# Kernel tuning notes

Measured on AMD Instinct MI355X. Metric: run time of the kernel, lower is better.

## Reference

```python
import jax, jax.numpy as jnp
import numpy as np

T = 24
ML = 10.0   # storage capacity constant `ml` from the repo
A_PEN = 10.0  # penalty weight `A`


def setup_inputs() -> dict:
    key = jax.random.key(0)
    k1, k2 = jax.random.split(key)
    B = 1 << 20
    out = jax.random.normal(k1, (B, T), dtype=jnp.float32)
    var_y = jax.random.normal(k2, (B, 2 * T), dtype=jnp.float32)
    return {"out": out, "var_y": var_y}


def _hinge(z):
    # (sign(z)+1)/2 * |z|  ==  max(z, 0) with torch's sign/abs grad semantics
    return (jnp.sign(z) + 1.0) * 0.5 * jnp.abs(z)


def reference(out, var_y):
    p = var_y[:, :T]          # prices  [B, T]
    a = var_y[:, T:]          # demand  [B, T]
    delta = out               # control [B, T]

    # recurrent state x0 after step t is cumsum(delta); at step t the loop
    # uses the *previous* x0 (0 at t=0)
    cum = jnp.cumsum(delta, axis=1)
    x0_prev = jnp.concatenate(
        [jnp.zeros_like(delta[:, :1]), cum[:, :-1]], axis=1)  # [B, T]

    # min_value_0 term only exists for t >= 1
    t_mask = (jnp.arange(T) >= 1).astype(delta.dtype)  # [T]

    min_v0 = _hinge(-delta - a) * t_mask
    max_v1 = _hinge(-delta - x0_prev)
    min_v1 = _hinge(x0_prev + delta - ML)

    pen = (min_v0 + max_v1 + min_v1) * A_PEN
    bill = jnp.abs(a + delta) * p + pen        # [B, T]
    # loop does cost += mean_over_batch(bill_t) for each t
    cost = jnp.sum(jnp.mean(bill, axis=0))
    return cost
```

## Files before the change

kernel.cpp:

```cpp
#include <hip/hip_runtime.h>


constexpr int TT = 24;
constexpr float ML_C = 10.0f;
constexpr float A_PEN_C = 10.0f;

__global__ __launch_bounds__(256)
void pen_partial_kernel(const float* __restrict__ dout,
                        const float* __restrict__ vary,
                        float* __restrict__ partial,
                        int B, float invB) {
    const int tid = threadIdx.x;
    const int row = blockIdx.x * 256 + tid;
    float s = 0.0f;
    if (row < B) {
        const float4* o4 = reinterpret_cast<const float4*>(dout + (size_t)row * TT);
        const float4* v4 = reinterpret_cast<const float4*>(vary + (size_t)row * (2 * TT));
        float d[TT], p[TT], a[TT];
        #pragma unroll
        for (int i = 0; i < TT / 4; ++i) {
            float4 t4 = o4[i];
            d[4*i+0] = t4.x; d[4*i+1] = t4.y; d[4*i+2] = t4.z; d[4*i+3] = t4.w;
        }
        #pragma unroll
        for (int i = 0; i < TT / 4; ++i) {
            float4 t4 = v4[i];
            p[4*i+0] = t4.x; p[4*i+1] = t4.y; p[4*i+2] = t4.z; p[4*i+3] = t4.w;
        }
        #pragma unroll
        for (int i = 0; i < TT / 4; ++i) {
            float4 t4 = v4[TT / 4 + i];
            a[4*i+0] = t4.x; a[4*i+1] = t4.y; a[4*i+2] = t4.z; a[4*i+3] = t4.w;
        }
        float x0 = 0.0f;
        #pragma unroll
        for (int t = 0; t < TT; ++t) {
            const float dd = d[t];
            const float aa = a[t];
            float mv0 = fmaxf(-dd - aa, 0.0f);
            if (t == 0) mv0 = 0.0f;
            const float mx1 = fmaxf(-dd - x0, 0.0f);
            const float mv1 = fmaxf(x0 + dd - ML_C, 0.0f);
            s += fabsf(aa + dd) * p[t] + (mv0 + mx1 + mv1) * A_PEN_C;
            x0 += dd;
        }
    }
    #pragma unroll
    for (int off = 32; off > 0; off >>= 1)
        s += __shfl_down(s, off, 64);
    __shared__ float ws[4];
    if ((tid & 63) == 0) ws[tid >> 6] = s;
    __syncthreads();
    if (tid == 0) {
        partial[blockIdx.x] = (ws[0] + ws[1] + ws[2] + ws[3]) * invB;
    }
}

__global__ __launch_bounds__(256)
void pen_final_reduce_kernel(const float* __restrict__ partial,
                             float* __restrict__ out, int n) {
    const int tid = threadIdx.x;
    float s = 0.0f;
    for (int i = tid; i < n; i += 256) s += partial[i];
    #pragma unroll
    for (int off = 32; off > 0; off >>= 1)
        s += __shfl_down(s, off, 64);
    __shared__ float ws[4];
    if ((tid & 63) == 0) ws[tid >> 6] = s;
    __syncthreads();
    if (tid == 0) out[0] = ws[0] + ws[1] + ws[2] + ws[3];
}

extern "C" void kernel_launch(void* const* d_in, const int* in_sizes, int n_in,
                              void* d_out, int out_size, void* d_ws, size_t ws_size,
                              hipStream_t stream) {
    const float* dout = (const float*)d_in[0];
    const float* vary = (const float*)d_in[1];
    const int B = in_sizes[0] / TT;
    const int nblocks = (B + 255) / 256;
    float* partial = (float*)d_ws;

    pen_partial_kernel<<<nblocks, 256, 0, stream>>>(dout, vary, partial, B, 1.0f / (float)B);
    pen_final_reduce_kernel<<<1, 256, 0, stream>>>(partial, (float*)d_out, nblocks);
}
```

Measured before the change: 340.3 us.

## Stage row tiles through padded LDS for coalesced global loads

Each block now handles 64 rows with one wavefront. It loads the rows cooperatively as contiguous float4 chunks into padded shared-memory tiles, then each thread reads its own row from LDS. Before, each thread read its own strided row directly from global memory. The goal is fully coalesced global reads in place of per-thread 96/192-byte strided accesses. The cost is LDS traffic and bank behaviour from the scalar stores at odd strides, plus 4x more blocks, which makes the single-block final reduction longer.

Result: no change. 345.5 us (+1.5%).

```diff
diff --git a/kernel.cpp b/kernel.cpp
--- a/kernel.cpp
+++ b/kernel.cpp
@@ -5,55 +5,85 @@
 constexpr float ML_C = 10.0f;
 constexpr float A_PEN_C = 10.0f;
 
-__global__ __launch_bounds__(256)
+constexpr int RPB  = 64;
+constexpr int DSTR = 25;
+constexpr int VSTR = 49;
+
+__global__ __launch_bounds__(64)
 void pen_partial_kernel(const float* __restrict__ dout,
                         const float* __restrict__ vary,
                         float* __restrict__ partial,
                         int B, float invB) {
+    __shared__ float ld[RPB * DSTR];
+    __shared__ float lv[RPB * VSTR];
     const int tid = threadIdx.x;
-    const int row = blockIdx.x * 256 + tid;
+    const long long rowBase = (long long)blockIdx.x * RPB;
+
     float s = 0.0f;
-    if (row < B) {
-        const float4* o4 = reinterpret_cast<const float4*>(dout + (size_t)row * TT);
-        const float4* v4 = reinterpret_cast<const float4*>(vary + (size_t)row * (2 * TT));
-        float d[TT], p[TT], a[TT];
+
+    if (rowBase + RPB <= B) {
+        const float4* g4 = reinterpret_cast<const float4*>(dout + rowBase * TT);
         #pragma unroll
-        for (int i = 0; i < TT / 4; ++i) {
-            float4 t4 = o4[i];
-            d[4*i+0] = t4.x; d[4*i+1] = t4.y; d[4*i+2] = t4.z; d[4*i+3] = t4.w;
+        for (int i = 0; i < 6; ++i) {
+            const int f = i * RPB + tid;
+            const float4 v = g4[f];
+            const int e = 4 * f;
+            const int r = e / TT;
+            const int c = e % TT;
+            float* dst = &ld[r * DSTR + c];
+            dst[0] = v.x; dst[1] = v.y; dst[2] = v.z; dst[3] = v.w;
         }
+        const float4* h4 = reinterpret_cast<const float4*>(vary + rowBase * (2 * TT));
         #pragma unroll
-        for (int i = 0; i < TT / 4; ++i) {
-            float4 t4 = v4[i];
-            p[4*i+0] = t4.x; p[4*i+1] = t4.y; p[4*i+2] = t4.z; p[4*i+3] = t4.w;
+        for (int i = 0; i < 12; ++i) {
+            const int f = i * RPB + tid;
+            const float4 v = h4[f];
+            const int e = 4 * f;
+            const int r = e / (2 * TT);
+            const int c = e % (2 * TT);
+            float* dst = &lv[r * VSTR + c];
+            dst[0] = v.x; dst[1] = v.y; dst[2] = v.z; dst[3] = v.w;
         }
-        #pragma unroll
-        for (int i = 0; i < TT / 4; ++i) {
-            float4 t4 = v4[TT / 4 + i];
-            a[4*i+0] = t4.x; a[4*i+1] = t4.y; a[4*i+2] = t4.z; a[4*i+3] = t4.w;
-        }
+        __syncthreads();
+
+        const float* drow = &ld[tid * DSTR];
+        const float* vrow = &lv[tid * VSTR];
         float x0 = 0.0f;
         #pragma unroll
         for (int t = 0; t < TT; ++t) {
-            const float dd = d[t];
-            const float aa = a[t];
+            const float dd = drow[t];
+            const float aa = vrow[TT + t];
+            const float pp = vrow[t];
             float mv0 = fmaxf(-dd - aa, 0.0f);
             if (t == 0) mv0 = 0.0f;
             const float mx1 = fmaxf(-dd - x0, 0.0f);
             const float mv1 = fmaxf(x0 + dd - ML_C, 0.0f);
-            s += fabsf(aa + dd) * p[t] + (mv0 + mx1 + mv1) * A_PEN_C;
+            s += fabsf(aa + dd) * pp + (mv0 + mx1 + mv1) * A_PEN_C;
             x0 += dd;
         }
+    } else {
+        const long long row = rowBase + tid;
+        if (row < B) {
+            const float* drow = dout + row * TT;
+            const float* vrow = vary + row * (2 * TT);
+            float x0 = 0.0f;
+            for (int t = 0; t < TT; ++t) {
+                const float dd = drow[t];
+                const float aa = vrow[TT + t];
+                float mv0 = fmaxf(-dd - aa, 0.0f);
+                if (t == 0) mv0 = 0.0f;
+                const float mx1 = fmaxf(-dd - x0, 0.0f);
+                const float mv1 = fmaxf(x0 + dd - ML_C, 0.0f);
+                s += fabsf(aa + dd) * vrow[t] + (mv0 + mx1 + mv1) * A_PEN_C;
+                x0 += dd;
+            }
+        }
     }
+
     #pragma unroll
     for (int off = 32; off > 0; off >>= 1)
         s += __shfl_down(s, off, 64);
-    __shared__ float ws[4];
-    if ((tid & 63) == 0) ws[tid >> 6] = s;
-    __syncthreads();
-    if (tid == 0) {
-        partial[blockIdx.x] = (ws[0] + ws[1] + ws[2] + ws[3]) * invB;
-    }
+    if (tid == 0) partial[blockIdx.x] = s * invB;
 }
 
 __global__ __launch_bounds__(256)
@@ -77,9 +107,9 @@
     const float* dout = (const float*)d_in[0];
     const float* vary = (const float*)d_in[1];
     const int B = in_sizes[0] / TT;
-    const int nblocks = (B + 255) / 256;
+    const int nblocks = (B + RPB - 1) / RPB;
     float* partial = (float*)d_ws;
 
-    pen_partial_kernel<<<nblocks, 256, 0, stream>>>(dout, vary, partial, B, 1.0f / (float)B);
+    pen_partial_kernel<<<nblocks, RPB, 0, stream>>>(dout, vary, partial, B, 1.0f / (float)B);
     pen_final_reduce_kernel<<<1, 256, 0, stream>>>(partial, (float*)d_out, nblocks);
 }
```

## Split each row across four lanes with shuffle prefix scan and grid-stride loop

Applied to the files above, without the earlier changes.

Each batch row is now handled by four lanes, six timesteps each. The lanes compute the prefix of cumulative control with a two-step shuffle scan, so a wavefront's global loads hit contiguous memory instead of 96-byte and 192-byte per-thread strides. The launch becomes a fixed 1024-block grid-stride loop that walks row groups in reverse order, which also cuts the number of partial sums the final reduce has to add. The cost is extra shuffles and the narrower float2 loads.

Measured after the change: 337.5 us. Within noise of the previous version (-0.8%).

```diff
diff --git a/kernel.cpp b/kernel.cpp
--- a/kernel.cpp
+++ b/kernel.cpp
@@ -5,54 +5,82 @@
 constexpr float ML_C = 10.0f;
 constexpr float A_PEN_C = 10.0f;
 
-__global__ __launch_bounds__(256)
+constexpr int LPR = 4;
+constexpr int EPL = 6;
+constexpr int RPW = 64 / LPR;
+constexpr int NBLK = 1024;
+constexpr int NTHR = 256;
+
+__global__ __launch_bounds__(NTHR)
 void pen_partial_kernel(const float* __restrict__ dout,
                         const float* __restrict__ vary,
                         float* __restrict__ partial,
                         int B, float invB) {
-    const int tid = threadIdx.x;
-    const int row = blockIdx.x * 256 + tid;
+    const int tid  = threadIdx.x;
+    const int lane = tid & 63;
+    const int sub  = lane & (LPR - 1);
+    const int g    = lane >> 2;
+
+    const int nWaves   = gridDim.x * (NTHR / 64);
+    const int waveId   = blockIdx.x * (NTHR / 64) + (tid >> 6);
+    const int RG       = (B + RPW - 1) / RPW;
+
     float s = 0.0f;
-    if (row < B) {
-        const float4* o4 = reinterpret_cast<const float4*>(dout + (size_t)row * TT);
-        const float4* v4 = reinterpret_cast<const float4*>(vary + (size_t)row * (2 * TT));
-        float d[TT], p[TT], a[TT];
+
+    for (int it = waveId; it < RG; it += nWaves) {
+        const int rg  = RG - 1 - it;
+        const long long row = (long long)rg * RPW + g;
+        if (row >= B) continue;
+
+        const float* dp = dout + row * TT + EPL * sub;
+        const float* vp = vary + row * (2 * TT) + EPL * sub;
+        const float* ap = vp + TT;
+        float2 d01 = *(const float2*)(dp);
+        float2 d23 = *(const float2*)(dp + 2);
+        float2 d45 = *(const float2*)(dp + 4);
+        float2 p01 = *(const float2*)(vp);
+        float2 p23 = *(const float2*)(vp + 2);
+        float2 p45 = *(const float2*)(vp + 4);
+        float2 a01 = *(const float2*)(ap);
+        float2 a23 = *(const float2*)(ap + 2);
+        float2 a45 = *(const float2*)(ap + 4);
+
+        float d[EPL] = {d01.x, d01.y, d23.x, d23.y, d45.x, d45.y};
+        float p[EPL] = {p01.x, p01.y, p23.x, p23.y, p45.x, p45.y};
+        float a[EPL] = {a01.x, a01.y, a23.x, a23.y, a45.x, a45.y};
+
+        const float localsum = ((d[0] + d[1]) + (d[2] + d[3])) + (d[4] + d[5]);
+        float incl = localsum;
+        float t1 = __shfl_up(incl, 1, LPR);
+        if (sub >= 1) incl += t1;
+        float t2 = __shfl_up(incl, 2, LPR);
+        if (sub >= 2) incl += t2;
+        float x0 = incl - localsum;
+
         #pragma unroll
-        for (int i = 0; i < TT / 4; ++i) {
-            float4 t4 = o4[i];
-            d[4*i+0] = t4.x; d[4*i+1] = t4.y; d[4*i+2] = t4.z; d[4*i+3] = t4.w;
-        }
-        #pragma unroll
-        for (int i = 0; i < TT / 4; ++i) {
-            float4 t4 = v4[i];
-            p[4*i+0] = t4.x; p[4*i+1] = t4.y; p[4*i+2] = t4.z; p[4*i+3] = t4.w;
-        }
-        #pragma unroll
-        for (int i = 0; i < TT / 4; ++i) {
-            float4 t4 = v4[TT / 4 + i];
-            a[4*i+0] = t4.x; a[4*i+1] = t4.y; a[4*i+2] = t4.z; a[4*i+3] = t4.w;
-        }
-        float x0 = 0.0f;
-        #pragma unroll
-        for (int t = 0; t < TT; ++t) {
-            const float dd = d[t];
-            const float aa = a[t];
+        for (int j = 0; j < EPL; ++j) {
+            const float dd = d[j];
+            const float aa = a[j];
             float mv0 = fmaxf(-dd - aa, 0.0f);
-            if (t == 0) mv0 = 0.0f;
+            if (j == 0 && sub == 0) mv0 = 0.0f;
             const float mx1 = fmaxf(-dd - x0, 0.0f);
             const float mv1 = fmaxf(x0 + dd - ML_C, 0.0f);
-            s += fabsf(aa + dd) * p[t] + (mv0 + mx1 + mv1) * A_PEN_C;
+            s += fabsf(aa + dd) * p[j] + (mv0 + mx1 + mv1) * A_PEN_C;
             x0 += dd;
         }
     }
+
     #pragma unroll
     for (int off = 32; off > 0; off >>= 1)
         s += __shfl_down(s, off, 64);
-    __shared__ float ws[4];
-    if ((tid & 63) == 0) ws[tid >> 6] = s;
+    __shared__ float ws[NTHR / 64];
+    if (lane == 0) ws[tid >> 6] = s;
     __syncthreads();
     if (tid == 0) {
-        partial[blockIdx.x] = (ws[0] + ws[1] + ws[2] + ws[3]) * invB;
+        float b = 0.0f;
+        #pragma unroll
+        for (int w = 0; w < NTHR / 64; ++w) b += ws[w];
+        partial[blockIdx.x] = b * invB;
     }
 }
 
@@ -77,9 +105,8 @@
     const float* dout = (const float*)d_in[0];
     const float* vary = (const float*)d_in[1];
     const int B = in_sizes[0] / TT;
-    const int nblocks = (B + 255) / 256;
     float* partial = (float*)d_ws;
 
-    pen_partial_kernel<<<nblocks, 256, 0, stream>>>(dout, vary, partial, B, 1.0f / (float)B);
-    pen_final_reduce_kernel<<<1, 256, 0, stream>>>(partial, (float*)d_out, nblocks);
+    pen_partial_kernel<<<NBLK, NTHR, 0, stream>>>(dout, vary, partial, B, 1.0f / (float)B);
+    pen_final_reduce_kernel<<<1, 256, 0, stream>>>(partial, (float*)d_out, NBLK);
 }
```
